# Performance work log

Measured on AMD Instinct MI355X. Metric: run time of the kernel, lower is better.

## Reference

```python
import jax, jax.numpy as jnp
import numpy as np

B, T, C, H = 16, 2048, 192, 64

def setup_inputs() -> dict:
    key = jax.random.key(0)
    k1, k2, k3, k4 = jax.random.split(key, 4)
    x = jax.random.normal(k1, (B, T, C), dtype=jnp.float32)
    Wq = jax.random.normal(k2, (C, H), dtype=jnp.float32) * (C ** -0.5)
    Wk = jax.random.normal(k3, (C, H), dtype=jnp.float32) * (C ** -0.5)
    Wv = jax.random.normal(k4, (C, H), dtype=jnp.float32) * (C ** -0.5)
    return {"x": x, "Wq": Wq, "Wk": Wk, "Wv": Wv}

def reference(x, Wq, Wk, Wv):
    # One head of causal self-attention (dropout in eval mode / identity).
    q = x @ Wq                       # [B, T, H]
    k = x @ Wk                       # [B, T, H]
    v = x @ Wv                       # [B, T, H]
    scale = q.shape[-1] ** -0.5
    wei = jnp.einsum('bth,bsh->bts', q, k) * scale   # [B, T, T]
    t = wei.shape[-1]
    causal = jnp.tril(jnp.ones((t, t), dtype=bool))  # tril mask
    wei = jnp.where(causal, wei, -jnp.inf)
    wei = jax.nn.softmax(wei, axis=-1)
    out = jnp.einsum('bts,bsh->bth', wei, v)         # [B, T, H]
    return out
```

## Files before the change

### kernel.cpp

```cpp
#include <hip/hip_runtime.h>

#define B 16
#define T 2048
#define C 192
#define H 64

typedef __bf16 bf16x8 __attribute__((ext_vector_type(8)));
typedef __bf16 bf16x4 __attribute__((ext_vector_type(4)));
typedef float  f32x4  __attribute__((ext_vector_type(4)));

#define MFMA(a, b, c) __builtin_amdgcn_mfma_f32_16x16x32_bf16(a, b, c, 0, 0, 0)

#define SM_BIAS 24.0f

__global__ __launch_bounds__(512) void qkv_mfma_kernel(
    const float* __restrict__ x,
    const float* __restrict__ Wq, const float* __restrict__ Wk,
    const float* __restrict__ Wv,
    __bf16* __restrict__ qb, __bf16* __restrict__ kb, __bf16* __restrict__ vt)
{
    __shared__ __bf16 Ws[192][200];
    __shared__ __bf16 tile[128][72];

    const int tid  = threadIdx.x;
    const int w    = tid >> 6;
    const int lid  = tid & 15;
    const int quad = (tid & 63) >> 4;
    const int m0   = blockIdx.x * 128 + w * 16;

    #pragma unroll
    for (int i = 0; i < 18; i++) {
        const int p = i * 512 + tid;
        const int m = p / 3072;
        const int r = p - m * 3072;
        const int k = r >> 4;
        const int nc4 = (r & 15) << 2;
        const float* W = (m == 0) ? Wq : (m == 1) ? Wk : Wv;
        const float4 v = *(const float4*)(W + k * H + nc4);
        const int n = m * 64 + nc4;
        Ws[n + 0][k] = (__bf16)v.x;
        Ws[n + 1][k] = (__bf16)v.y;
        Ws[n + 2][k] = (__bf16)v.z;
        Ws[n + 3][k] = (__bf16)v.w;
    }

    const float* xrow = x + (size_t)(m0 + lid) * C + quad * 8;
    bf16x8 af[6];
    #pragma unroll
    for (int kc = 0; kc < 6; kc++) {
        const float4 a0 = *(const float4*)(xrow + kc * 32);
        const float4 a1 = *(const float4*)(xrow + kc * 32 + 4);
        af[kc][0] = (__bf16)a0.x; af[kc][1] = (__bf16)a0.y;
        af[kc][2] = (__bf16)a0.z; af[kc][3] = (__bf16)a0.w;
        af[kc][4] = (__bf16)a1.x; af[kc][5] = (__bf16)a1.y;
        af[kc][6] = (__bf16)a1.z; af[kc][7] = (__bf16)a1.w;
    }
    __syncthreads();

    f32x4 acc[12] = {};
    #pragma unroll
    for (int kc = 0; kc < 6; kc++)
        #pragma unroll
        for (int nt = 0; nt < 12; nt++) {
            const bf16x8 bfr =
                *(const bf16x8*)&Ws[nt * 16 + lid][kc * 32 + quad * 8];
            acc[nt] = MFMA(af[kc], bfr, acc[nt]);
        }

    #pragma unroll
    for (int nt = 0; nt < 8; nt++) {
        const int n = nt * 16 + lid;
        __bf16* dst = (n < 64) ? qb : kb;
        const int col = n & 63;
        const float scale = (n < 64) ? 0.1803368801111204f : 1.0f;
        #pragma unroll
        for (int r = 0; r < 4; r++) {
            const int row = m0 + quad * 4 + r;
            dst[(size_t)row * H + col] = (__bf16)(acc[nt][r] * scale);
        }
    }

    #pragma unroll
    for (int nt = 8; nt < 12; nt++) {
        const int col = (nt - 8) * 16 + lid;
        #pragma unroll
        for (int r = 0; r < 4; r++)
            tile[w * 16 + quad * 4 + r][col] = (__bf16)(acc[nt][r]);
    }
    __syncthreads();

    const int bb = blockIdx.x >> 4;
    const int t0 = (blockIdx.x & 15) << 7;
    #pragma unroll
    for (int it = 0; it < 2; ++it) {
        const int q   = it * 512 + tid;
        const int h   = q >> 4;
        const int tl0 = (q & 15) * 8;
        const int base32 = tl0 & ~31;
        const int qq = (tl0 >> 3) & 3;
        bf16x8 d;
        #pragma unroll
        for (int j = 0; j < 8; j++) {
            const int key = base32 + qq * 4 + (j < 4 ? j : j + 12);
            d[j] = tile[key][h];
        }
        *(bf16x8*)(vt + ((size_t)(bb * H + h)) * T + t0 + tl0) = d;
    }
}

__global__ __launch_bounds__(512, 4) void attn_kernel(
    const __bf16* __restrict__ qb,
    const __bf16* __restrict__ kb,
    const __bf16* __restrict__ vt,
    float* __restrict__ out)
{
    __shared__ __bf16 Kb[2][2][64][72];
    __shared__ __bf16 Vb[2][2][64][72];

    const int tid  = threadIdx.x;
    const int wv   = tid >> 6;
    const int grp  = wv >> 2;
    const int w    = wv & 3;
    const int lid  = tid & 15;
    const int quad = (tid & 63) >> 4;

    const int half = blockIdx.x >> 8;
    const int rem  = blockIdx.x & 255;
    const int b    = rem & 15;
    const int pr   = rem >> 4;
    const int qt   = half ? pr : (31 - pr);
    const int nch  = qt + 1;
    const int nsteps = (nch + 1) >> 1;
    const size_t bbase = (size_t)b * T;

    const int qX = (qt << 6) + w * 16;

    const __bf16* qr = qb + (bbase + qX + lid) * H + quad * 8;
    const bf16x8 qf0 = *(const bf16x8*)(qr);
    const bf16x8 qf1 = *(const bf16x8*)(qr + 32);

    const __bf16* kgb = kb + bbase * H;
    const __bf16* vgb = vt + (size_t)b * H * T;

    const int ra = tid >> 3, ca = (tid & 7) * 8;

    auto keyof = [&](int i) {
        if (i > nch - 1) i = nch - 1;
        return i << 6;
    };

    auto prefetchInto = [&](bf16x8 (&kr)[2], bf16x8 (&vr)[2], int s) {
        #pragma unroll
        for (int g = 0; g < 2; g++) {
            const int key0 = keyof(2 * s + g);
            kr[g] = *(const bf16x8*)(kgb + (size_t)(key0 + ra) * H + ca);
            vr[g] = *(const bf16x8*)(vgb + (size_t)ra * T + key0 + ca);
        }
    };

    f32x4 O[4] = {};
    f32x4 lsv = {0.f, 0.f, 0.f, 0.f};

    auto doChunk = [&](int key0, int cur) {
        const __bf16 (*Kc)[72] = Kb[cur][grp];
        const __bf16 (*Vc)[72] = Vb[cur][grp];
        bf16x8 af0, af1;
        const bool boundary = (key0 + 63 > qX);
        #pragma unroll
        for (int j = 0; j < 4; j++) {
            const __bf16* kp = &Kc[j * 16 + lid][quad * 8];
            const bf16x8 kf0 = *(const bf16x8*)(kp);
            const bf16x8 kf1 = *(const bf16x8*)(kp + 32);
            f32x4 sS = {-SM_BIAS, -SM_BIAS, -SM_BIAS, -SM_BIAS};
            sS = MFMA(kf0, qf0, sS);
            sS = MFMA(kf1, qf1, sS);
            if (boundary) {
                #pragma unroll
                for (int r = 0; r < 4; r++)
                    if (key0 + j * 16 + quad * 4 + r > qX + lid) sS[r] = -1e30f;
            }
            #pragma unroll
            for (int r = 0; r < 4; r++) {
                const float p = __builtin_amdgcn_exp2f(sS[r]);
                lsv[r] += p;
                if      (j == 0) af0[r]     = (__bf16)p;
                else if (j == 1) af0[4 + r] = (__bf16)p;
                else if (j == 2) af1[r]     = (__bf16)p;
                else             af1[4 + r] = (__bf16)p;
            }
        }
        #pragma unroll
        for (int ht = 0; ht < 4; ht++) {
            const __bf16* vp = &Vc[ht * 16 + lid][quad * 8];
            const bf16x8 bv0 = *(const bf16x8*)(vp);
            const bf16x8 bv1 = *(const bf16x8*)(vp + 32);
            O[ht] = MFMA(af0, bv0, O[ht]);
            O[ht] = MFMA(af1, bv1, O[ht]);
        }
    };

    auto stageWrite = [&](int cur, bf16x8 (&kr)[2], bf16x8 (&vr)[2]) {
        *(bf16x8*)&Kb[cur][0][ra][ca] = kr[0];
        *(bf16x8*)&Kb[cur][1][ra][ca] = kr[1];
        *(bf16x8*)&Vb[cur][0][ra][ca] = vr[0];
        *(bf16x8*)&Vb[cur][1][ra][ca] = vr[1];
    };

    bf16x8 krA[2], vrA[2], krB[2], vrB[2];
    int cur = 0;

    prefetchInto(krA, vrA, 0);
    for (int s = 0; s < nsteps; s += 2) {
        if (s + 1 < nsteps) prefetchInto(krB, vrB, s + 1);
        stageWrite(cur, krA, vrA);
        __syncthreads();
        {
            const int i = 2 * s + grp;
            if (i < nch) doChunk(i << 6, cur);
        }
        cur ^= 1;
        if (s + 1 >= nsteps) break;
        if (s + 2 < nsteps) prefetchInto(krA, vrA, s + 2);
        stageWrite(cur, krB, vrB);
        __syncthreads();
        {
            const int i = 2 * (s + 1) + grp;
            if (i < nch) doChunk(i << 6, cur);
        }
        cur ^= 1;
    }

    __syncthreads();
    float* sO = (float*)&Kb[0][0][0][0];
    float* sL = (float*)&Vb[0][0][0][0];

    float l = lsv[0] + lsv[1] + lsv[2] + lsv[3];
    l += __shfl_xor(l, 16, 64);
    l += __shfl_xor(l, 32, 64);

    if (grp == 1) {
        #pragma unroll
        for (int ht = 0; ht < 4; ht++)
            #pragma unroll
            for (int r = 0; r < 4; r++)
                sO[(w * 16 + quad * 4 + r) * 64 + ht * 16 + lid] = O[ht][r];
        if ((tid & 63) < 16) sL[w * 16 + lid] = l;
    }
    __syncthreads();
    if (grp == 0) {
        l += sL[w * 16 + lid];
        #pragma unroll
        for (int ht = 0; ht < 4; ht++)
            #pragma unroll
            for (int r = 0; r < 4; r++) {
                const float Lr = __shfl(l, quad * 4 + r, 16);
                const float v = O[ht][r]
                    + sO[(w * 16 + quad * 4 + r) * 64 + ht * 16 + lid];
                out[(bbase + qX + quad * 4 + r) * H + ht * 16 + lid] = v / Lr;
            }
    }
}

extern "C" void kernel_launch(void* const* d_in, const int* in_sizes, int n_in,
                              void* d_out, int out_size, void* d_ws, size_t ws_size,
                              hipStream_t stream)
{
    const float* x  = (const float*)d_in[0];
    const float* Wq = (const float*)d_in[1];
    const float* Wk = (const float*)d_in[2];
    const float* Wv = (const float*)d_in[3];

    const size_t BTH = (size_t)B * T * H;
    __bf16* qbuf = (__bf16*)d_ws;
    __bf16* kbuf = qbuf + BTH;
    __bf16* vtb  = kbuf + BTH;
    float* outp = (float*)d_out;

    qkv_mfma_kernel<<<B * T / 128, 512, 0, stream>>>(x, Wq, Wk, Wv,
                                                     qbuf, kbuf, vtb);
    attn_kernel<<<B * T / 128 * 2, 512, 0, stream>>>(qbuf, kbuf, vtb, outp);
}
```

Measured before the change: 101.6 us.

## Merge paired causal query tiles into one 1024-thread block sharing K/V staging

New measurement: 101.9 us. No clear change (+0.2%).

```diff
diff --git a/kernel.cpp b/kernel.cpp
--- a/kernel.cpp
+++ b/kernel.cpp
@@ -108,7 +108,7 @@
     }
 }
 
-__global__ __launch_bounds__(512, 4) void attn_kernel(
+__global__ __launch_bounds__(1024, 4) void attn_kernel(
     const __bf16* __restrict__ qb,
     const __bf16* __restrict__ kb,
     const __bf16* __restrict__ vt,
@@ -119,18 +119,19 @@
 
     const int tid  = threadIdx.x;
     const int wv   = tid >> 6;
-    const int grp  = wv >> 2;
+    const int tle  = wv >> 3;
+    const int grp  = (wv >> 2) & 1;
     const int w    = wv & 3;
     const int lid  = tid & 15;
     const int quad = (tid & 63) >> 4;
 
-    const int half = blockIdx.x >> 8;
-    const int rem  = blockIdx.x & 255;
-    const int b    = rem & 15;
-    const int pr   = rem >> 4;
-    const int qt   = half ? pr : (31 - pr);
+    const int b    = blockIdx.x & 15;
+    const int pr   = blockIdx.x >> 4;
+    const int qtH  = 31 - pr;
+    const int nchH = qtH + 1;
+    const int qt   = tle ? pr : qtH;
     const int nch  = qt + 1;
-    const int nsteps = (nch + 1) >> 1;
+    const int nsteps = (nchH + 1) >> 1;
     const size_t bbase = (size_t)b * T;
 
     const int qX = (qt << 6) + w * 16;
@@ -142,19 +143,33 @@
     const __bf16* kgb = kb + bbase * H;
     const __bf16* vgb = vt + (size_t)b * H * T;
 
-    const int ra = tid >> 3, ca = (tid & 7) * 8;
+    const int sr   = tid & 511;
+    const int ra   = sr >> 3;
+    const int ca   = (sr & 7) * 8;
+    const bool stK = (tid < 512);
 
     auto keyof = [&](int i) {
-        if (i > nch - 1) i = nch - 1;
+        if (i > nchH - 1) i = nchH - 1;
         return i << 6;
     };
 
-    auto prefetchInto = [&](bf16x8 (&kr)[2], bf16x8 (&vr)[2], int s) {
+    auto prefetchInto = [&](bf16x8 (&rg)[2], int s) {
         #pragma unroll
         for (int g = 0; g < 2; g++) {
             const int key0 = keyof(2 * s + g);
-            kr[g] = *(const bf16x8*)(kgb + (size_t)(key0 + ra) * H + ca);
-            vr[g] = *(const bf16x8*)(vgb + (size_t)ra * T + key0 + ca);
+            rg[g] = stK
+                ? *(const bf16x8*)(kgb + (size_t)(key0 + ra) * H + ca)
+                : *(const bf16x8*)(vgb + (size_t)ra * T + key0 + ca);
+        }
+    };
+
+    auto stageWrite = [&](int cur, bf16x8 (&rg)[2]) {
+        if (stK) {
+            *(bf16x8*)&Kb[cur][0][ra][ca] = rg[0];
+            *(bf16x8*)&Kb[cur][1][ra][ca] = rg[1];
+        } else {
+            *(bf16x8*)&Vb[cur][0][ra][ca] = rg[0];
+            *(bf16x8*)&Vb[cur][1][ra][ca] = rg[1];
         }
     };
 
@@ -199,20 +214,13 @@
         }
     };
 
-    auto stageWrite = [&](int cur, bf16x8 (&kr)[2], bf16x8 (&vr)[2]) {
-        *(bf16x8*)&Kb[cur][0][ra][ca] = kr[0];
-        *(bf16x8*)&Kb[cur][1][ra][ca] = kr[1];
-        *(bf16x8*)&Vb[cur][0][ra][ca] = vr[0];
-        *(bf16x8*)&Vb[cur][1][ra][ca] = vr[1];
-    };
-
-    bf16x8 krA[2], vrA[2], krB[2], vrB[2];
+    bf16x8 rA[2], rB[2];
     int cur = 0;
 
-    prefetchInto(krA, vrA, 0);
+    prefetchInto(rA, 0);
     for (int s = 0; s < nsteps; s += 2) {
-        if (s + 1 < nsteps) prefetchInto(krB, vrB, s + 1);
-        stageWrite(cur, krA, vrA);
+        if (s + 1 < nsteps) prefetchInto(rB, s + 1);
+        stageWrite(cur, rA);
         __syncthreads();
         {
             const int i = 2 * s + grp;
@@ -220,8 +228,8 @@
         }
         cur ^= 1;
         if (s + 1 >= nsteps) break;
-        if (s + 2 < nsteps) prefetchInto(krA, vrA, s + 2);
-        stageWrite(cur, krB, vrB);
+        if (s + 2 < nsteps) prefetchInto(rA, s + 2);
+        stageWrite(cur, rB);
         __syncthreads();
         {
             const int i = 2 * (s + 1) + grp;
@@ -243,19 +251,21 @@
         for (int ht = 0; ht < 4; ht++)
             #pragma unroll
             for (int r = 0; r < 4; r++)
-                sO[(w * 16 + quad * 4 + r) * 64 + ht * 16 + lid] = O[ht][r];
-        if ((tid & 63) < 16) sL[w * 16 + lid] = l;
+                sO[tle * 4096 + (w * 16 + quad * 4 + r) * 64 + ht * 16 + lid] =
+                    O[ht][r];
+        if ((tid & 63) < 16) sL[tle * 64 + w * 16 + lid] = l;
     }
     __syncthreads();
     if (grp == 0) {
-        l += sL[w * 16 + lid];
+        l += sL[tle * 64 + w * 16 + lid];
         #pragma unroll
         for (int ht = 0; ht < 4; ht++)
             #pragma unroll
             for (int r = 0; r < 4; r++) {
                 const float Lr = __shfl(l, quad * 4 + r, 16);
                 const float v = O[ht][r]
-                    + sO[(w * 16 + quad * 4 + r) * 64 + ht * 16 + lid];
+                    + sO[tle * 4096 + (w * 16 + quad * 4 + r) * 64 +
+                         ht * 16 + lid];
                 out[(bbase + qX + quad * 4 + r) * H + ht * 16 + lid] = v / Lr;
             }
     }
@@ -278,5 +288,5 @@
 
     qkv_mfma_kernel<<<B * T / 128, 512, 0, stream>>>(x, Wq, Wk, Wv,
                                                      qbuf, kbuf, vtb);
-    attn_kernel<<<B * T / 128 * 2, 512, 0, stream>>>(qbuf, kbuf, vtb, outp);
+    attn_kernel<<<B * T / 128, 1024, 0, stream>>>(qbuf, kbuf, vtb, outp);
 }
```
